# Optimization experiments

Measured on AMD Instinct MI355X. Metric: run time of the kernel, lower is better.

## Reference

```python
import jax, jax.numpy as jnp
import numpy as np

NUM_NODES = 100000
EMBED_DIM = 64
NUM_LAYERS = 3
NUM_EDGES = 3200000


def setup_inputs() -> dict:
    key = jax.random.key(0)
    k1, k2 = jax.random.split(key)
    # xavier_uniform for [N, D]: bound = sqrt(6/(N+D))
    bound = float(np.sqrt(6.0 / (NUM_NODES + EMBED_DIM)))
    emb = jax.random.uniform(k1, (NUM_NODES, EMBED_DIM), dtype=jnp.float32,
                             minval=-bound, maxval=bound)
    edge_index = jax.random.randint(k2, (2, NUM_EDGES), 0, NUM_NODES, dtype=jnp.int64)
    return {"emb": emb, "edge_index": edge_index}


def reference(emb, edge_index):
    # LightGCN: xs = [x0, LGConv(x0), LGConv^2(x0), ...]; output = mean(xs)
    # LGConv (PyG, add_self_loops=False): out[i] = sum_{(j,i) in E} x[j] / sqrt(d_j * d_i)
    n = emb.shape[0]
    row, col = edge_index[0], edge_index[1]  # row = source j, col = target i
    ones = jnp.ones(row.shape[0], dtype=emb.dtype)
    deg = jax.ops.segment_sum(ones, col, num_segments=n)  # in-degree per gcn_norm
    dinv = jnp.where(deg > 0, jax.lax.rsqrt(jnp.where(deg > 0, deg, 1.0)), 0.0)
    norm = dinv[row] * dinv[col]  # [E]

    x = emb
    acc = emb
    for _ in range(NUM_LAYERS):
        msgs = x[row] * norm[:, None]                      # gather + normalize [E, D]
        x = jax.ops.segment_sum(msgs, col, num_segments=n)  # scatter-add [N, D]
        acc = acc + x
    return acc / (NUM_LAYERS + 1)
```

## Files before the change

### kernel.cpp

```cpp
#include <hip/hip_runtime.h>
#include <hip/hip_bf16.h>
#include <hip/hip_fp16.h>
#include <stdint.h>


#define N_NODES 100000
#define N_EDGES 3200000
#define DIM 64

#define BSH 9
#define BNODES 512
#define NB 196
#define CAP 20480

#define CHUNK 8192
#define NBLK1 ((N_EDGES + CHUNK - 1) / CHUNK)

__global__ __launch_bounds__(256) void k_bucket(const int* __restrict__ ei,
                                                int* __restrict__ gcursor,
                                                int* __restrict__ staging) {
    __shared__ int stage[CHUNK];
    __shared__ unsigned char sbkt[CHUNK];
    __shared__ int bcnt[2][NB];
    __shared__ int boff[NB];
    __shared__ int bstart[NB];
    __shared__ int gbase[NB];
    __shared__ int wt[4];

    int t = threadIdx.x;
    int e0 = blockIdx.x * CHUNK;
    int nblk = min(CHUNK, N_EDGES - e0);
    int nvec = nblk >> 2;

    const int4* col4 = (const int4*)(ei + N_EDGES + e0);
    const int4* row4 = (const int4*)(ei + e0);

    for (int i = t; i < NB; i += 256) { bcnt[0][i] = 0; bcnt[1][i] = 0; boff[i] = 0; }
    __syncthreads();

    int rep = t & 1;
    for (int i = t; i < nvec; i += 256) {
        int4 c = col4[i];
        atomicAdd(&bcnt[rep][c.x >> BSH], 1);
        atomicAdd(&bcnt[rep][c.y >> BSH], 1);
        atomicAdd(&bcnt[rep][c.z >> BSH], 1);
        atomicAdd(&bcnt[rep][c.w >> BSH], 1);
    }
    __syncthreads();

    {
        int v = (t < NB) ? (bcnt[0][t] + bcnt[1][t]) : 0;
        int lane = t & 63, w = t >> 6;
        int s = v;
#pragma unroll
        for (int off = 1; off < 64; off <<= 1) {
            int u = __shfl_up(s, off);
            if (lane >= off) s += u;
        }
        if (lane == 63) wt[w] = s;
        __syncthreads();
        int wo = 0;
        for (int ww = 0; ww < w; ww++) wo += wt[ww];
        if (t < NB) {
            bstart[t] = s - v + wo;
            gbase[t] = (v > 0) ? atomicAdd(&gcursor[t], v) : 0;
        }
    }
    __syncthreads();

    for (int i = t; i < nvec; i += 256) {
        int4 c = col4[i];
        int4 r = row4[i];
        int b0 = c.x >> BSH, b1 = c.y >> BSH, b2 = c.z >> BSH, b3 = c.w >> BSH;
        int p0 = bstart[b0] + atomicAdd(&boff[b0], 1);
        int p1 = bstart[b1] + atomicAdd(&boff[b1], 1);
        int p2 = bstart[b2] + atomicAdd(&boff[b2], 1);
        int p3 = bstart[b3] + atomicAdd(&boff[b3], 1);
        stage[p0] = (r.x << BSH) | (c.x & (BNODES - 1)); sbkt[p0] = (unsigned char)b0;
        stage[p1] = (r.y << BSH) | (c.y & (BNODES - 1)); sbkt[p1] = (unsigned char)b1;
        stage[p2] = (r.z << BSH) | (c.z & (BNODES - 1)); sbkt[p2] = (unsigned char)b2;
        stage[p3] = (r.w << BSH) | (c.w & (BNODES - 1)); sbkt[p3] = (unsigned char)b3;
    }
    __syncthreads();

    for (int i = t; i < nblk; i += 256) {
        int e = stage[i];
        int b = sbkt[i];
        staging[(size_t)b * CAP + gbase[b] + (i - bstart[b])] = e;
    }
}

__global__ __launch_bounds__(256) void k_build(const int* __restrict__ gcursor,
                                               const int* __restrict__ staging,
                                               int4* __restrict__ rec,
                                               float* __restrict__ dinv,
                                               int* __restrict__ csrc) {
    __shared__ int ldeg[BNODES];
    __shared__ int lcur[BNODES];
    __shared__ int gsc[NB];
    __shared__ int wtt[4];

    int b = blockIdx.x >> 2;
    int q = blockIdx.x & 3;
    int t = threadIdx.x;
    int n0 = b << BSH;
    int nloc = min(BNODES, N_NODES - n0);
    int cnt = gcursor[b];
    const int* st = staging + (size_t)b * CAP;

    {
        int v = (t < NB) ? gcursor[t] : 0;
        int lane = t & 63, w = t >> 6;
        int ss = v;
#pragma unroll
        for (int off = 1; off < 64; off <<= 1) {
            int u = __shfl_up(ss, off);
            if (lane >= off) ss += u;
        }
        if (lane == 63) wtt[w] = ss;
        ldeg[t] = 0; ldeg[t + 256] = 0;
        __syncthreads();
        int wo = 0;
        for (int ww = 0; ww < w; ww++) wo += wtt[ww];
        if (t < NB) gsc[t] = ss - v + wo;
    }
    __syncthreads();
    int bstartB = gsc[b];

    for (int i = t; i < cnt; i += 256) {
        atomicAdd(&ldeg[st[i] & (BNODES - 1)], 1);
    }
    __syncthreads();

    int a0 = ldeg[2 * t], a1 = ldeg[2 * t + 1];
    int s = a0 + a1;
    int lane = t & 63, w = t >> 6;
    int ss = s;
#pragma unroll
    for (int off = 1; off < 64; off <<= 1) {
        int u = __shfl_up(ss, off);
        if (lane >= off) ss += u;
    }
    if (lane == 63) wtt[w] = ss;
    __syncthreads();
    int wo = 0;
    for (int ww = 0; ww < w; ww++) wo += wtt[ww];
    int excl = ss - s + wo;

    int gb = bstartB + excl;
    int n = n0 + 2 * t;
    lcur[2 * t] = gb;
    lcur[2 * t + 1] = gb + a0;
    if (((2 * t) >> 7) == q) {
        if (2 * t < nloc) {
            float di = (a0 > 0) ? rsqrtf((float)a0) : 0.0f;
            rec[n] = make_int4(gb, a0, __float_as_int(di), 0);
            dinv[n] = di;
        }
        if (2 * t + 1 < nloc) {
            float di = (a1 > 0) ? rsqrtf((float)a1) : 0.0f;
            rec[n + 1] = make_int4(gb + a0, a1, __float_as_int(di), 0);
            dinv[n + 1] = di;
        }
    }
    __syncthreads();

    for (int i = t; i < cnt; i += 256) {
        int e = st[i];
        int dl = e & (BNODES - 1);
        if ((dl >> 7) == q) {
            int p = atomicAdd(&lcur[dl], 1);
            csrc[p] = e >> BSH;
        }
    }
}

__global__ void k_z0(const float* __restrict__ emb, const float* __restrict__ dinv,
                     __half* __restrict__ zA, __half* __restrict__ zB) {
    const int total = (N_NODES * DIM) / 4;
    int i = blockIdx.x * blockDim.x + threadIdx.x;
    if (i >= total) {
        int r = i - total;
        if (r < 16) ((uint2*)(zA + (size_t)N_NODES * DIM))[r] = make_uint2(0, 0);
        else if (r < 32) ((uint2*)(zB + (size_t)N_NODES * DIM))[r - 16] = make_uint2(0, 0);
        return;
    }
    float di = dinv[(i * 4) >> 6];
    const float4 v = ((const float4*)emb)[i];
    union { ushort h[4]; uint2 u; } pk;
    __half h0 = __float2half(v.x * di);
    __half h1 = __float2half(v.y * di);
    __half h2 = __float2half(v.z * di);
    __half h3 = __float2half(v.w * di);
    pk.h[0] = *(ushort*)&h0; pk.h[1] = *(ushort*)&h1;
    pk.h[2] = *(ushort*)&h2; pk.h[3] = *(ushort*)&h3;
    ((uint2*)zA)[i] = pk.u;
}

__global__ __launch_bounds__(256) void k_spmv(
    const int4* __restrict__ rec, const int* __restrict__ csrc,
    const __half* __restrict__ z, __half* __restrict__ znext,
    const __half* __restrict__ zprev, const float* __restrict__ emb,
    float* __restrict__ out, int mode) {
    int wave = (blockIdx.x * blockDim.x + threadIdx.x) >> 6;
    int lane = threadIdx.x & 63;
    if (wave >= N_NODES) return;
    int g = lane >> 3;
    int l = lane & 7;

    int4 nr = rec[wave];
    int start = nr.x;
    int cnt = nr.y;
    float di = __int_as_float(nr.z);
    int ng = (cnt + 7) >> 3;

    __half2 hz = __float2half2_rn(0.0f);
    __half2 hacc0 = hz, hacc1 = hz, hacc2 = hz, hacc3 = hz;

#define GIDX(KK, SV)                                 \
    int e_##SV = (KK) * 8 + g;                       \
    int SV = csrc[start + e_##SV];                   \
    SV = (e_##SV < cnt) ? SV : N_NODES;

#define GFETCH(SV, VV)                               \
    uint4 VV = *((const uint4*)(z + ((size_t)SV << 6)) + l);

#define GADD(VV)                                                          \
    do {                                                                  \
        const __half2* hv = (const __half2*)&VV;                          \
        hacc0 = __hadd2(hacc0, hv[0]);                                    \
        hacc1 = __hadd2(hacc1, hv[1]);                                    \
        hacc2 = __hadd2(hacc2, hv[2]);                                    \
        hacc3 = __hadd2(hacc3, hv[3]);                                    \
    } while (0)

    int k = 0;
    for (; k + 4 <= ng; k += 4) {
        GIDX(k + 0, s0) GIDX(k + 1, s1) GIDX(k + 2, s2) GIDX(k + 3, s3)
        GFETCH(s0, v0) GFETCH(s1, v1) GFETCH(s2, v2) GFETCH(s3, v3)
        GADD(v0); GADD(v1); GADD(v2); GADD(v3);
    }
    int rem = ng - k;
    if (rem > 0) {
        GIDX(k + 0, t0)
        if (rem > 1) {
            GIDX(k + 1, t1)
            if (rem > 2) {
                GIDX(k + 2, t2)
                GFETCH(t0, w0) GFETCH(t1, w1) GFETCH(t2, w2)
                GADD(w0); GADD(w1); GADD(w2);
            } else {
                GFETCH(t0, w0) GFETCH(t1, w1)
                GADD(w0); GADD(w1);
            }
        } else {
            GFETCH(t0, w0)
            GADD(w0);
        }
    }
#undef GIDX
#undef GFETCH
#undef GADD

#pragma unroll
    for (int off = 8; off <= 32; off <<= 1) {
        int b0 = __shfl_xor(*(int*)&hacc0, off);
        int b1 = __shfl_xor(*(int*)&hacc1, off);
        int b2 = __shfl_xor(*(int*)&hacc2, off);
        int b3 = __shfl_xor(*(int*)&hacc3, off);
        hacc0 = __hadd2(hacc0, *(__half2*)&b0);
        hacc1 = __hadd2(hacc1, *(__half2*)&b1);
        hacc2 = __hadd2(hacc2, *(__half2*)&b2);
        hacc3 = __hadd2(hacc3, *(__half2*)&b3);
    }

    if (lane < 8) {
        size_t o = (size_t)wave * DIM + lane * 8;
        float x[8];
        x[0] = __low2float(hacc0) * di; x[1] = __high2float(hacc0) * di;
        x[2] = __low2float(hacc1) * di; x[3] = __high2float(hacc1) * di;
        x[4] = __low2float(hacc2) * di; x[5] = __high2float(hacc2) * di;
        x[6] = __low2float(hacc3) * di; x[7] = __high2float(hacc3) * di;

        if (mode == 0) {
            union { ushort h[8]; uint4 u; } pk;
#pragma unroll
            for (int j = 0; j < 8; j++) {
                __half hh = __float2half(x[j] * di);
                pk.h[j] = *(ushort*)&hh;
            }
            *((uint4*)(znext + o)) = pk.u;
        } else {
            float sdeg = (cnt > 0) ? sqrtf((float)cnt) : 0.0f;
            uint4 v2 = *((const uint4*)(zprev + o));
            uint4 v3 = *((const uint4*)(z + o));
            const __half2* h2 = (const __half2*)&v2;
            const __half2* h3 = (const __half2*)&v3;
            float4 e0 = ((const float4*)(emb + o))[0];
            float4 e1 = ((const float4*)(emb + o))[1];
            float zs[8];
#pragma unroll
            for (int j = 0; j < 4; j++) {
                float2 a2 = __half22float2(h2[j]);
                float2 a3 = __half22float2(h3[j]);
                zs[2 * j] = a2.x + a3.x;
                zs[2 * j + 1] = a2.y + a3.y;
            }
            float4 o0 = make_float4(
                (e0.x + sdeg * zs[0] + x[0]) * 0.25f,
                (e0.y + sdeg * zs[1] + x[1]) * 0.25f,
                (e0.z + sdeg * zs[2] + x[2]) * 0.25f,
                (e0.w + sdeg * zs[3] + x[3]) * 0.25f);
            float4 o1 = make_float4(
                (e1.x + sdeg * zs[4] + x[4]) * 0.25f,
                (e1.y + sdeg * zs[5] + x[5]) * 0.25f,
                (e1.z + sdeg * zs[6] + x[6]) * 0.25f,
                (e1.w + sdeg * zs[7] + x[7]) * 0.25f);
            ((float4*)(out + o))[0] = o0;
            ((float4*)(out + o))[1] = o1;
        }
    }
}

extern "C" void kernel_launch(void* const* d_in, const int* in_sizes, int n_in,
                              void* d_out, int out_size, void* d_ws, size_t ws_size,
                              hipStream_t stream) {
    const float* emb = (const float*)d_in[0];
    const int* ei = (const int*)d_in[1];
    float* out = (float*)d_out;

    char* ws = (char*)d_ws;
    size_t off = 0;
    auto alloc = [&](size_t bytes) -> void* {
        void* p = ws + off;
        off += (bytes + 511) & ~(size_t)511;
        return p;
    };
    int4* rec = (int4*)alloc((size_t)N_NODES * 16);
    float* dinv = (float*)alloc((size_t)N_NODES * 4);
    int* gcursor = (int*)alloc(NB * 4);
    int* csrc = (int*)alloc(((size_t)N_EDGES + 64) * 4);
    size_t zbytes = (size_t)(N_NODES + 1) * DIM * 2;
    size_t stbytes = (size_t)NB * CAP * 4;
    char* transient = (char*)alloc(stbytes > zbytes ? stbytes : zbytes);
    int* staging = (int*)transient;
    __half* zA = (__half*)transient;
    __half* zB = (__half*)alloc(zbytes);

    hipMemsetAsync(gcursor, 0, NB * 4, stream);

    k_bucket<<<NBLK1, 256, 0, stream>>>(ei, gcursor, staging);
    k_build<<<NB * 4, 256, 0, stream>>>(gcursor, staging, rec, dinv, csrc);
    k_z0<<<(N_NODES * DIM / 4) / 256 + 1, 256, 0, stream>>>(emb, dinv, zA, zB);

    int spmvBlocks = (N_NODES + 3) / 4;
    k_spmv<<<spmvBlocks, 256, 0, stream>>>(rec, csrc, zA, zB, nullptr, emb, out, 0);
    k_spmv<<<spmvBlocks, 256, 0, stream>>>(rec, csrc, zB, zA, nullptr, emb, out, 0);
    k_spmv<<<spmvBlocks, 256, 0, stream>>>(rec, csrc, zA, nullptr, zB, emb, out, 2);
}
```

Before: 313.0 us.

## Fuse z0 scaling into CSR build and restrict build blocks to their quarter

Folds the separate z0 kernel, which scales embeddings by inverse degree and converts them to half, into the CSR build kernel, so the dinv array and one launch go away. Each build block now counts degrees only for its own 128-node quarter and gets the quarter offset from a ballot-based count, which cuts the shared-memory atomics that every block used to repeat for all 512 nodes. zA and zB swap buffers so zA no longer aliases staging while k_build writes it, and padding rows are zeroed with memsets. The bucket kernel also drops its two-copy histogram, which may raise shared-atomic contention.

```diff
diff --git a/kernel.cpp b/kernel.cpp
--- a/kernel.cpp
+++ b/kernel.cpp
@@ -21,7 +21,7 @@
                                                 int* __restrict__ staging) {
     __shared__ int stage[CHUNK];
     __shared__ unsigned char sbkt[CHUNK];
-    __shared__ int bcnt[2][NB];
+    __shared__ int bcnt[NB];
     __shared__ int boff[NB];
     __shared__ int bstart[NB];
     __shared__ int gbase[NB];
@@ -35,21 +35,20 @@
     const int4* col4 = (const int4*)(ei + N_EDGES + e0);
     const int4* row4 = (const int4*)(ei + e0);
 
-    for (int i = t; i < NB; i += 256) { bcnt[0][i] = 0; bcnt[1][i] = 0; boff[i] = 0; }
-    __syncthreads();
-
-    int rep = t & 1;
+    for (int i = t; i < NB; i += 256) { bcnt[i] = 0; boff[i] = 0; }
+    __syncthreads();
+
     for (int i = t; i < nvec; i += 256) {
         int4 c = col4[i];
-        atomicAdd(&bcnt[rep][c.x >> BSH], 1);
-        atomicAdd(&bcnt[rep][c.y >> BSH], 1);
-        atomicAdd(&bcnt[rep][c.z >> BSH], 1);
-        atomicAdd(&bcnt[rep][c.w >> BSH], 1);
+        atomicAdd(&bcnt[c.x >> BSH], 1);
+        atomicAdd(&bcnt[c.y >> BSH], 1);
+        atomicAdd(&bcnt[c.z >> BSH], 1);
+        atomicAdd(&bcnt[c.w >> BSH], 1);
     }
     __syncthreads();
 
     {
-        int v = (t < NB) ? (bcnt[0][t] + bcnt[1][t]) : 0;
+        int v = (t < NB) ? bcnt[t] : 0;
         int lane = t & 63, w = t >> 6;
         int s = v;
 #pragma unroll
@@ -92,25 +91,29 @@
 
 __global__ __launch_bounds__(256) void k_build(const int* __restrict__ gcursor,
                                                const int* __restrict__ staging,
+                                               const float* __restrict__ emb,
                                                int4* __restrict__ rec,
-                                               float* __restrict__ dinv,
-                                               int* __restrict__ csrc) {
-    __shared__ int ldeg[BNODES];
-    __shared__ int lcur[BNODES];
+                                               int* __restrict__ csrc,
+                                               __half* __restrict__ zA) {
+    __shared__ int ldeg[128];
+    __shared__ int lcur[128];
     __shared__ int gsc[NB];
+    __shared__ int qcnt[4];
     __shared__ int wtt[4];
 
     int b = blockIdx.x >> 2;
     int q = blockIdx.x & 3;
     int t = threadIdx.x;
-    int n0 = b << BSH;
-    int nloc = min(BNODES, N_NODES - n0);
+    int lane = t & 63, w = t >> 6;
+    int n0 = (b << BSH) + (q << 7);
     int cnt = gcursor[b];
     const int* st = staging + (size_t)b * CAP;
 
+    if (t < 128) ldeg[t] = 0;
+    if (t < 4) qcnt[t] = 0;
+
     {
         int v = (t < NB) ? gcursor[t] : 0;
-        int lane = t & 63, w = t >> 6;
         int ss = v;
 #pragma unroll
         for (int off = 1; off < 64; off <<= 1) {
@@ -118,24 +121,34 @@
             if (lane >= off) ss += u;
         }
         if (lane == 63) wtt[w] = ss;
-        ldeg[t] = 0; ldeg[t + 256] = 0;
         __syncthreads();
         int wo = 0;
         for (int ww = 0; ww < w; ww++) wo += wtt[ww];
         if (t < NB) gsc[t] = ss - v + wo;
     }
     __syncthreads();
-    int bstartB = gsc[b];
-
-    for (int i = t; i < cnt; i += 256) {
-        atomicAdd(&ldeg[st[i] & (BNODES - 1)], 1);
-    }
-    __syncthreads();
-
-    int a0 = ldeg[2 * t], a1 = ldeg[2 * t + 1];
-    int s = a0 + a1;
-    int lane = t & 63, w = t >> 6;
-    int ss = s;
+
+    int iters = (cnt + 255) >> 8;
+    for (int it = 0; it < iters; it++) {
+        int i = it * 256 + t;
+        bool valid = i < cnt;
+        int e = valid ? st[i] : 0;
+        int dl = e & (BNODES - 1);
+        int qq = dl >> 7;
+#pragma unroll
+        for (int z = 0; z < 4; z++) {
+            unsigned long long m = __ballot(valid && qq == z);
+            if (lane == 0 && m) atomicAdd(&qcnt[z], __popcll(m));
+        }
+        if (valid && qq == q) atomicAdd(&ldeg[dl & 127], 1);
+    }
+    __syncthreads();
+
+    int qpre = 0;
+    for (int z = 0; z < q; z++) qpre += qcnt[z];
+
+    int a = (t < 128) ? ldeg[t] : 0;
+    int ss = a;
 #pragma unroll
     for (int off = 1; off < 64; off <<= 1) {
         int u = __shfl_up(ss, off);
@@ -145,22 +158,15 @@
     __syncthreads();
     int wo = 0;
     for (int ww = 0; ww < w; ww++) wo += wtt[ww];
-    int excl = ss - s + wo;
-
-    int gb = bstartB + excl;
-    int n = n0 + 2 * t;
-    lcur[2 * t] = gb;
-    lcur[2 * t + 1] = gb + a0;
-    if (((2 * t) >> 7) == q) {
-        if (2 * t < nloc) {
-            float di = (a0 > 0) ? rsqrtf((float)a0) : 0.0f;
-            rec[n] = make_int4(gb, a0, __float_as_int(di), 0);
-            dinv[n] = di;
-        }
-        if (2 * t + 1 < nloc) {
-            float di = (a1 > 0) ? rsqrtf((float)a1) : 0.0f;
-            rec[n + 1] = make_int4(gb + a0, a1, __float_as_int(di), 0);
-            dinv[n + 1] = di;
+    int excl = ss - a + wo;
+
+    if (t < 128) {
+        int gb = gsc[b] + qpre + excl;
+        lcur[t] = gb;
+        int n = n0 + t;
+        if (n < N_NODES) {
+            float di = (a > 0) ? rsqrtf((float)a) : 0.0f;
+            rec[n] = make_int4(gb, a, __float_as_int(di), 0);
         }
     }
     __syncthreads();
@@ -169,32 +175,28 @@
         int e = st[i];
         int dl = e & (BNODES - 1);
         if ((dl >> 7) == q) {
-            int p = atomicAdd(&lcur[dl], 1);
+            int p = atomicAdd(&lcur[dl & 127], 1);
             csrc[p] = e >> BSH;
         }
     }
-}
-
-__global__ void k_z0(const float* __restrict__ emb, const float* __restrict__ dinv,
-                     __half* __restrict__ zA, __half* __restrict__ zB) {
-    const int total = (N_NODES * DIM) / 4;
-    int i = blockIdx.x * blockDim.x + threadIdx.x;
-    if (i >= total) {
-        int r = i - total;
-        if (r < 16) ((uint2*)(zA + (size_t)N_NODES * DIM))[r] = make_uint2(0, 0);
-        else if (r < 32) ((uint2*)(zB + (size_t)N_NODES * DIM))[r - 16] = make_uint2(0, 0);
-        return;
-    }
-    float di = dinv[(i * 4) >> 6];
-    const float4 v = ((const float4*)emb)[i];
-    union { ushort h[4]; uint2 u; } pk;
-    __half h0 = __float2half(v.x * di);
-    __half h1 = __float2half(v.y * di);
-    __half h2 = __float2half(v.z * di);
-    __half h3 = __float2half(v.w * di);
-    pk.h[0] = *(ushort*)&h0; pk.h[1] = *(ushort*)&h1;
-    pk.h[2] = *(ushort*)&h2; pk.h[3] = *(ushort*)&h3;
-    ((uint2*)zA)[i] = pk.u;
+
+    for (int i = t; i < 128 * (DIM / 4); i += 256) {
+        int nl = i >> 4;
+        int n = n0 + nl;
+        if (n < N_NODES) {
+            int d = ldeg[nl];
+            float di = (d > 0) ? rsqrtf((float)d) : 0.0f;
+            const float4 v = ((const float4*)(emb + (size_t)n * DIM))[i & 15];
+            union { ushort h[4]; uint2 u; } pk;
+            __half h0 = __float2half(v.x * di);
+            __half h1 = __float2half(v.y * di);
+            __half h2 = __float2half(v.z * di);
+            __half h3 = __float2half(v.w * di);
+            pk.h[0] = *(ushort*)&h0; pk.h[1] = *(ushort*)&h1;
+            pk.h[2] = *(ushort*)&h2; pk.h[3] = *(ushort*)&h3;
+            ((uint2*)(zA + (size_t)n * DIM))[i & 15] = pk.u;
+        }
+    }
 }
 
 __global__ __launch_bounds__(256) void k_spmv(
@@ -337,21 +339,21 @@
         return p;
     };
     int4* rec = (int4*)alloc((size_t)N_NODES * 16);
-    float* dinv = (float*)alloc((size_t)N_NODES * 4);
     int* gcursor = (int*)alloc(NB * 4);
     int* csrc = (int*)alloc(((size_t)N_EDGES + 64) * 4);
     size_t zbytes = (size_t)(N_NODES + 1) * DIM * 2;
     size_t stbytes = (size_t)NB * CAP * 4;
     char* transient = (char*)alloc(stbytes > zbytes ? stbytes : zbytes);
     int* staging = (int*)transient;
-    __half* zA = (__half*)transient;
-    __half* zB = (__half*)alloc(zbytes);
+    __half* zB = (__half*)transient;
+    __half* zA = (__half*)alloc(zbytes);
 
     hipMemsetAsync(gcursor, 0, NB * 4, stream);
+    hipMemsetAsync(zA + (size_t)N_NODES * DIM, 0, DIM * 2, stream);
 
     k_bucket<<<NBLK1, 256, 0, stream>>>(ei, gcursor, staging);
-    k_build<<<NB * 4, 256, 0, stream>>>(gcursor, staging, rec, dinv, csrc);
-    k_z0<<<(N_NODES * DIM / 4) / 256 + 1, 256, 0, stream>>>(emb, dinv, zA, zB);
+    k_build<<<NB * 4, 256, 0, stream>>>(gcursor, staging, emb, rec, csrc, zA);
+    hipMemsetAsync(zB + (size_t)N_NODES * DIM, 0, DIM * 2, stream);
 
     int spmvBlocks = (N_NODES + 3) / 4;
     k_spmv<<<spmvBlocks, 256, 0, stream>>>(rec, csrc, zA, zB, nullptr, emb, out, 0);
```

New measurement: 337.1 us. 7.7% more time.
